# Kernel tuning notes

Hardware: AMD Instinct MI355X
Metric: run time of the kernel (lower is better)

The kernel has to match this reference:

```python
import jax, jax.numpy as jnp
import numpy as np

B, N_IN, N_HID, N_OUT = 4096, 1024, 4096, 1024

def setup_inputs() -> dict:
    key = jax.random.key(0)
    k_x, k_w1, k_b1, k_w2, k_b2 = jax.random.split(key, 5)
    # Per-node LiveNet weights, batched: each hidden neuron = relu(sum_i w_i * in_i + b),
    # each output neuron = linear sum over hidden neurons.
    s1 = 1.0 / np.sqrt(N_IN)
    s2 = 1.0 / np.sqrt(N_HID)
    return {
        "x": jax.random.normal(k_x, (B, N_IN), dtype=jnp.float32),
        "W1": jax.random.uniform(k_w1, (N_IN, N_HID), jnp.float32, -s1, s1),
        "b1": jax.random.uniform(k_b1, (N_HID,), jnp.float32, -s1, s1),
        "W2": jax.random.uniform(k_w2, (N_HID, N_OUT), jnp.float32, -s2, s2),
        "b2": jax.random.uniform(k_b2, (N_OUT,), jnp.float32, -s2, s2),
    }

def reference(x, W1, b1, W2, b2):
    # Batched equivalent of LiveNet's per-node traversal:
    # inputs[i].set_output(x[:, i:i+1]); each hidden neuron computes
    # relu(weighted sum of parents + bias); each output node is a linear
    # weighted sum of hidden outputs; outputs concatenated along dim=1.
    h = jax.nn.relu(x @ W1 + b1)          # [B, N_HID]
    y = h @ W2 + b2                        # [B, N_OUT]
    return y
```

## Files before the change

### kernel.cpp

```cpp
#include <hip/hip_runtime.h>
#include <stdint.h>

#define BDIM  4096
#define NIN   1024
#define NHID  4096
#define NOUT  1024

typedef unsigned short u16;
typedef unsigned int   u32;
typedef __attribute__((ext_vector_type(8))) __bf16 bf16x8;
typedef __attribute__((ext_vector_type(4))) float  f32x4;

__device__ __forceinline__ u16 f32_to_bf16_rne(float f) {
    u32 u = __builtin_bit_cast(u32, f);
    u = (u + 0x7fffu + ((u >> 16) & 1u)) >> 16;
    return (u16)u;
}

__device__ __forceinline__ void transpose_tile(
    const float* __restrict__ in, u16* __restrict__ out,
    int R, int C, int bx, int by, float (*tile)[33]) {
    const int rt = by * 32, ct = bx * 32;
    const int tid = threadIdx.x;
    {
        const int r  = tid >> 3;
        const int c4 = (tid & 7) * 4;
        float4 v = *(const float4*)(in + (size_t)(rt + r) * C + ct + c4);
        tile[r][c4 + 0] = v.x; tile[r][c4 + 1] = v.y;
        tile[r][c4 + 2] = v.z; tile[r][c4 + 3] = v.w;
    }
    __syncthreads();
    if (tid < 128) {
        const int oc = tid >> 2;
        const int ch = tid & 3;
        u16 tmp[8];
#pragma unroll
        for (int j = 0; j < 8; ++j)
            tmp[j] = f32_to_bf16_rne(tile[ch * 8 + j][oc]);
        u16* dst = out + (size_t)(ct + oc) * R + rt + ch * 8;
        ushort4 lo = {tmp[0], tmp[1], tmp[2], tmp[3]};
        ushort4 hi = {tmp[4], tmp[5], tmp[6], tmp[7]};
        *(ushort4*)dst = lo;
        *(ushort4*)(dst + 4) = hi;
    }
}

__global__ void prepass(const float* __restrict__ x,  u16* __restrict__ x_bf,
                        const float* __restrict__ W1, u16* __restrict__ W1t,
                        const float* __restrict__ W2, u16* __restrict__ W2t) {
    __shared__ float tile[32][33];
    const int b = blockIdx.x;
    if (b < 4096) {
        int i = b * 256 + threadIdx.x;
        float4 v = ((const float4*)x)[i];
        ushort4 o;
        o.x = f32_to_bf16_rne(v.x); o.y = f32_to_bf16_rne(v.y);
        o.z = f32_to_bf16_rne(v.z); o.w = f32_to_bf16_rne(v.w);
        ((ushort4*)x_bf)[i] = o;
    } else if (b < 8192) {
        int t = b - 4096;
        transpose_tile(W1, W1t, NIN, NHID, t & 127, t >> 7, tile);
    } else {
        int t = b - 8192;
        transpose_tile(W2, W2t, NHID, NOUT, t & 31, t >> 5, tile);
    }
}

__global__ __launch_bounds__(512) void gemm_bt_relu(
    const u16* __restrict__ A, const u16* __restrict__ Bt,
    const float* __restrict__ bias, u16* __restrict__ outp,
    int M, int N, int K)
{
    constexpr int MI = 4, NI = 4;
    __shared__ __align__(16) u16 smemA[256 * 64];
    __shared__ __align__(16) u16 smemB[128 * 64];

    const int bid = blockIdx.x;
    const int cxcd = bid & 7;
    const int j    = bid >> 3;
    const int bx   = ((cxcd & 3) << 3) + (j & 7);
    const int by   = ((cxcd >> 2) << 3) + (j >> 3);

    const int tid  = threadIdx.x;
    const int lane = tid & 63;
    const int wave = tid >> 6;
    const int rowBase = by * 256;
    const int colBase = bx * 128;
    const int wrow = (wave >> 1) * 64;
    const int wcol = (wave & 1) * 64;

    f32x4 acc[MI][NI] = {};

    const int srow    = lane >> 3;
    const int chunkSw = (lane & 7) ^ srow;
    const int gcol    = chunkSw * 8;
    const int fr = lane & 15;
    const int fq = lane >> 4;
    const int sw = fr & 7;

    for (int k0 = 0; k0 < K; k0 += 64) {
        __syncthreads();
#pragma unroll
        for (int t = 0; t < 4; ++t) {
            int region = wave * 4 + t;
            int arow = rowBase + region * 8 + srow;
            const u16* g = A + (size_t)arow * K + k0 + gcol;
            __builtin_amdgcn_global_load_lds(
                (const __attribute__((address_space(1))) u32*)g,
                (__attribute__((address_space(3))) u32*)(smemA + region * 512),
                16, 0, 0);
        }
#pragma unroll
        for (int t = 0; t < 2; ++t) {
            int region = wave * 2 + t;
            int brow = colBase + region * 8 + srow;
            const u16* g = Bt + (size_t)brow * K + k0 + gcol;
            __builtin_amdgcn_global_load_lds(
                (const __attribute__((address_space(1))) u32*)g,
                (__attribute__((address_space(3))) u32*)(smemB + region * 512),
                16, 0, 0);
        }
        __builtin_amdgcn_s_waitcnt(0);
        __syncthreads();

#pragma unroll
        for (int s = 0; s < 2; ++s) {
            const int co = ((s * 4 + fq) ^ sw) * 16;
            const char* aB = (const char*)smemA + (wrow + fr) * 128 + co;
            const char* bB = (const char*)smemB + (wcol + fr) * 128 + co;
            bf16x8 af[MI], bfv[NI];
#pragma unroll
            for (int mi = 0; mi < MI; ++mi)
                af[mi] = *(const bf16x8*)(aB + mi * 2048);
#pragma unroll
            for (int ni = 0; ni < NI; ++ni)
                bfv[ni] = *(const bf16x8*)(bB + ni * 2048);
#pragma unroll
            for (int mi = 0; mi < MI; ++mi)
#pragma unroll
                for (int ni = 0; ni < NI; ++ni)
                    acc[mi][ni] = __builtin_amdgcn_mfma_f32_16x16x32_bf16(
                        af[mi], bfv[ni], acc[mi][ni], 0, 0, 0);
        }
    }

    const int col0 = colBase + wcol + fr;
    const int row0 = rowBase + wrow + (fq << 2);
#pragma unroll
    for (int ni = 0; ni < NI; ++ni) {
        const int col = col0 + ni * 16;
        const float bv = bias[col];
#pragma unroll
        for (int mi = 0; mi < MI; ++mi) {
            const int row = row0 + mi * 16;
#pragma unroll
            for (int r = 0; r < 4; ++r) {
                float v = acc[mi][ni][r] + bv;
                v = v > 0.f ? v : 0.f;
                outp[(size_t)(row + r) * N + col] = f32_to_bf16_rne(v);
            }
        }
    }
}

__global__ __launch_bounds__(256) void gemm2_splitk(
    const u16* __restrict__ A, const u16* __restrict__ Bt,
    float* __restrict__ out0, float* __restrict__ p1,
    int M, int N, int K, int Kchunk)
{
    constexpr int MI = 4, NI = 4;
    __shared__ __align__(16) u16 smemA[128 * 64];
    __shared__ __align__(16) u16 smemB[128 * 64];

    const int bid = blockIdx.x;
    const int cxcd = bid & 7;
    const int j    = bid >> 3;
    const int z    = cxcd >> 2;
    const int bx   = j & 7;
    const int by   = ((cxcd & 3) << 3) + (j >> 3);

    const int tid  = threadIdx.x;
    const int lane = tid & 63;
    const int wave = tid >> 6;
    const int rowBase = by * 128;
    const int colBase = bx * 128;
    const int kBeg = z * Kchunk;
    const int kEnd = kBeg + Kchunk;
    const int wrow = (wave >> 1) * 64;
    const int wcol = (wave & 1) * 64;

    f32x4 acc[MI][NI] = {};

    const int srow    = lane >> 3;
    const int chunkSw = (lane & 7) ^ srow;
    const int gcol    = chunkSw * 8;
    const int fr = lane & 15;
    const int fq = lane >> 4;
    const int sw = fr & 7;

    for (int k0 = kBeg; k0 < kEnd; k0 += 64) {
        __syncthreads();
#pragma unroll
        for (int t = 0; t < 4; ++t) {
            int region = wave * 4 + t;
            int arow = rowBase + region * 8 + srow;
            const u16* g = A + (size_t)arow * K + k0 + gcol;
            __builtin_amdgcn_global_load_lds(
                (const __attribute__((address_space(1))) u32*)g,
                (__attribute__((address_space(3))) u32*)(smemA + region * 512),
                16, 0, 0);
        }
#pragma unroll
        for (int t = 0; t < 4; ++t) {
            int region = wave * 4 + t;
            int brow = colBase + region * 8 + srow;
            const u16* g = Bt + (size_t)brow * K + k0 + gcol;
            __builtin_amdgcn_global_load_lds(
                (const __attribute__((address_space(1))) u32*)g,
                (__attribute__((address_space(3))) u32*)(smemB + region * 512),
                16, 0, 0);
        }
        __builtin_amdgcn_s_waitcnt(0);
        __syncthreads();

#pragma unroll
        for (int s = 0; s < 2; ++s) {
            const int co = ((s * 4 + fq) ^ sw) * 16;
            const char* aB = (const char*)smemA + (wrow + fr) * 128 + co;
            const char* bB = (const char*)smemB + (wcol + fr) * 128 + co;
            bf16x8 af[MI], bfv[NI];
#pragma unroll
            for (int mi = 0; mi < MI; ++mi)
                af[mi] = *(const bf16x8*)(aB + mi * 2048);
#pragma unroll
            for (int ni = 0; ni < NI; ++ni)
                bfv[ni] = *(const bf16x8*)(bB + ni * 2048);
#pragma unroll
            for (int mi = 0; mi < MI; ++mi)
#pragma unroll
                for (int ni = 0; ni < NI; ++ni)
                    acc[mi][ni] = __builtin_amdgcn_mfma_f32_16x16x32_bf16(
                        af[mi], bfv[ni], acc[mi][ni], 0, 0, 0);
        }
    }

    float* outp = (z == 0) ? out0 : p1;
    const int col0 = colBase + wcol + fr;
    const int row0 = rowBase + wrow + (fq << 2);
#pragma unroll
    for (int ni = 0; ni < NI; ++ni) {
        const int col = col0 + ni * 16;
#pragma unroll
        for (int mi = 0; mi < MI; ++mi) {
            const int row = row0 + mi * 16;
#pragma unroll
            for (int r = 0; r < 4; ++r)
                outp[(size_t)(row + r) * N + col] = acc[mi][ni][r];
        }
    }
}

__global__ void splitk_reduce(float* __restrict__ out0,
                              const float* __restrict__ p,
                              const float* __restrict__ bias,
                              int n4, int nCols4) {
    int i = blockIdx.x * blockDim.x + threadIdx.x;
    if (i >= n4) return;
    float4 v = ((const float4*)out0)[i];
    float4 q = ((const float4*)p)[i];
    float4 bv = ((const float4*)bias)[i & (nCols4 - 1)];
    v.x += q.x + bv.x; v.y += q.y + bv.y;
    v.z += q.z + bv.z; v.w += q.w + bv.w;
    ((float4*)out0)[i] = v;
}

extern "C" void kernel_launch(void* const* d_in, const int* in_sizes, int n_in,
                              void* d_out, int out_size, void* d_ws, size_t ws_size,
                              hipStream_t stream) {
    const float* x  = (const float*)d_in[0];
    const float* W1 = (const float*)d_in[1];
    const float* b1 = (const float*)d_in[2];
    const float* W2 = (const float*)d_in[3];
    const float* b2 = (const float*)d_in[4];

    char* ws = (char*)d_ws;
    const size_t MB = 1024 * 1024;
    u16*   W2t  = (u16*)(ws + 0 * MB);
    u16*   h_bf = (u16*)(ws + 8 * MB);
    u16*   x_bf = (u16*)(ws + 40 * MB);
    u16*   W1t  = (u16*)(ws + 48 * MB);
    float* p1   = (float*)(ws + 56 * MB);

    prepass<<<12288, 256, 0, stream>>>(x, x_bf, W1, W1t, W2, W2t);

    gemm_bt_relu<<<512, 512, 0, stream>>>(
        x_bf, W1t, b1, h_bf, BDIM, NHID, NIN);

    gemm2_splitk<<<512, 256, 0, stream>>>(
        h_bf, W2t, (float*)d_out, p1, BDIM, NOUT, NHID, NHID / 2);

    int rn4 = BDIM * NOUT / 4;
    splitk_reduce<<<(rn4 + 255) / 256, 256, 0, stream>>>(
        (float*)d_out, p1, b2, rn4, NOUT / 4);
}
```

Measured before the change: 180.8 us.

## Enlarge GEMM2 tile to 256x128 with split-K of four and fold bias into epilogue

The second GEMM now uses 512-thread blocks computing 256x128 output tiles, and K is split four ways instead of two so the grid stays at 512 blocks. The bias add moves into the z==0 epilogue, and the reduce kernel sums three partial buffers with no bias lookup. The aim is more operand reuse per block from the taller A tile and a shorter K loop per block. The cost is two extra fp32 partial buffers of the full output size that must be written and then read back in the reduce pass, which adds global memory traffic.

```diff
diff --git a/kernel.cpp b/kernel.cpp
--- a/kernel.cpp
+++ b/kernel.cpp
@@ -163,26 +163,26 @@
     }
 }
 
-__global__ __launch_bounds__(256) void gemm2_splitk(
+__global__ __launch_bounds__(512) void gemm2_splitk(
     const u16* __restrict__ A, const u16* __restrict__ Bt,
-    float* __restrict__ out0, float* __restrict__ p1,
-    int M, int N, int K, int Kchunk)
+    const float* __restrict__ bias, float* __restrict__ out0,
+    float* __restrict__ pextra, int M, int N, int K, int Kchunk)
 {
     constexpr int MI = 4, NI = 4;
-    __shared__ __align__(16) u16 smemA[128 * 64];
+    __shared__ __align__(16) u16 smemA[256 * 64];
     __shared__ __align__(16) u16 smemB[128 * 64];
 
     const int bid = blockIdx.x;
     const int cxcd = bid & 7;
     const int j    = bid >> 3;
-    const int z    = cxcd >> 2;
+    const int z    = cxcd >> 1;
     const int bx   = j & 7;
-    const int by   = ((cxcd & 3) << 3) + (j >> 3);
+    const int by   = ((cxcd & 1) << 3) + (j >> 3);
 
     const int tid  = threadIdx.x;
     const int lane = tid & 63;
     const int wave = tid >> 6;
-    const int rowBase = by * 128;
+    const int rowBase = by * 256;
     const int colBase = bx * 128;
     const int kBeg = z * Kchunk;
     const int kEnd = kBeg + Kchunk;
@@ -211,8 +211,8 @@
                 16, 0, 0);
         }
 #pragma unroll
-        for (int t = 0; t < 4; ++t) {
-            int region = wave * 4 + t;
+        for (int t = 0; t < 2; ++t) {
+            int region = wave * 2 + t;
             int brow = colBase + region * 8 + srow;
             const u16* g = Bt + (size_t)brow * K + k0 + gcol;
             __builtin_amdgcn_global_load_lds(
@@ -244,33 +244,35 @@
         }
     }
 
-    float* outp = (z == 0) ? out0 : p1;
+    float* outp = (z == 0) ? out0 : (pextra + (size_t)(z - 1) * M * N);
     const int col0 = colBase + wcol + fr;
     const int row0 = rowBase + wrow + (fq << 2);
 #pragma unroll
     for (int ni = 0; ni < NI; ++ni) {
         const int col = col0 + ni * 16;
+        const float bv = (z == 0) ? bias[col] : 0.f;
 #pragma unroll
         for (int mi = 0; mi < MI; ++mi) {
             const int row = row0 + mi * 16;
 #pragma unroll
             for (int r = 0; r < 4; ++r)
-                outp[(size_t)(row + r) * N + col] = acc[mi][ni][r];
+                outp[(size_t)(row + r) * N + col] = acc[mi][ni][r] + bv;
         }
     }
 }
 
 __global__ void splitk_reduce(float* __restrict__ out0,
-                              const float* __restrict__ p,
-                              const float* __restrict__ bias,
-                              int n4, int nCols4) {
+                              const float* __restrict__ pextra,
+                              int n4) {
     int i = blockIdx.x * blockDim.x + threadIdx.x;
     if (i >= n4) return;
     float4 v = ((const float4*)out0)[i];
-    float4 q = ((const float4*)p)[i];
-    float4 bv = ((const float4*)bias)[i & (nCols4 - 1)];
-    v.x += q.x + bv.x; v.y += q.y + bv.y;
-    v.z += q.z + bv.z; v.w += q.w + bv.w;
+    const size_t s4 = (size_t)n4;
+#pragma unroll
+    for (int s = 0; s < 3; ++s) {
+        float4 p = ((const float4*)pextra)[i + s * s4];
+        v.x += p.x; v.y += p.y; v.z += p.z; v.w += p.w;
+    }
     ((float4*)out0)[i] = v;
 }
 
@@ -289,17 +291,17 @@
     u16*   h_bf = (u16*)(ws + 8 * MB);
     u16*   x_bf = (u16*)(ws + 40 * MB);
     u16*   W1t  = (u16*)(ws + 48 * MB);
-    float* p1   = (float*)(ws + 56 * MB);
+    float* pex  = (float*)(ws + 56 * MB);
 
     prepass<<<12288, 256, 0, stream>>>(x, x_bf, W1, W1t, W2, W2t);
 
     gemm_bt_relu<<<512, 512, 0, stream>>>(
         x_bf, W1t, b1, h_bf, BDIM, NHID, NIN);
 
-    gemm2_splitk<<<512, 256, 0, stream>>>(
-        h_bf, W2t, (float*)d_out, p1, BDIM, NOUT, NHID, NHID / 2);
+    gemm2_splitk<<<512, 512, 0, stream>>>(
+        h_bf, W2t, b2, (float*)d_out, pex, BDIM, NOUT, NHID, NHID / 4);
 
     int rn4 = BDIM * NOUT / 4;
     splitk_reduce<<<(rn4 + 255) / 256, 256, 0, stream>>>(
-        (float*)d_out, p1, b2, rn4, NOUT / 4);
-}
+        (float*)d_out, pex, rn4);
+}
```

Result: no change. 183.2 us (+1.3%).
